# Optimization experiments

Hardware: AMD Instinct MI355X
Metric: run time of the kernel (lower is better)

The kernel has to match this reference:

```python
import jax, jax.numpy as jnp
import numpy as np

B, M, TP2, H, K, S = 64, 1, 1024, 256, 128, 1024
EPS = 2.220446049250313e-16  # numpy.finfo(float).eps


def setup_inputs() -> dict:
    key = jax.random.key(0)
    ks = jax.random.split(key, 12)
    inp = {
        'event': jax.random.randint(ks[0], (B, M, TP2), 0, K + 3),
        'dtime': jax.random.uniform(ks[1], (B, M, TP2), jnp.float32),
        'post': jax.random.uniform(ks[2], (B, M), jnp.float32),
        'duration': jax.random.uniform(ks[3], (B, M), jnp.float32),
        'dtime_sampling': jax.random.uniform(ks[4], (B, M, S), jnp.float32),
        'index_of_hidden_sampling': jax.random.randint(ks[5], (B, M, S), 0, B * M * (TP2 - 1)),
        'mask_sampling': jnp.ones((B, M, S), jnp.float32),
        # learned parameters
        'Emb': jax.random.normal(ks[6], (K + 3, H), jnp.float32) * 0.05,
        'W': jax.random.normal(ks[7], (7 * H, 2 * H), jnp.float32) * (1.0 / np.sqrt(2 * H)),
        'b': jnp.zeros((7 * H,), jnp.float32),
        'Wl': jax.random.normal(ks[8], (K, H), jnp.float32) * (1.0 / np.sqrt(H)),
    }
    return inp


def reference(event, dtime, post, duration, dtime_sampling, index_of_hidden_sampling,
              mask_sampling, Emb, W, b, Wl):
    Bs, Ms, Tp2 = event.shape
    Hd = Emb.shape[1]
    Tp1 = Tp2 - 1
    emb = Emb[event[:, :, :-1]]            # (B,M,T+1,H)
    dts = dtime[:, :, 1:]                  # (B,M,T+1)
    xs = (jnp.moveaxis(emb, 2, 0), jnp.moveaxis(dts, 2, 0))

    def step(carry, x):
        h, c, cbar = carry
        e, dt = x
        z = jnp.concatenate([e, h], axis=-1) @ W.T + b  # (B,M,7H)
        gi, gf, go, gz, gib, gfb, gd = jnp.split(z, 7, axis=-1)
        gi, gf, go = jax.nn.sigmoid(gi), jax.nn.sigmoid(gf), jax.nn.sigmoid(go)
        gib, gfb = jax.nn.sigmoid(gib), jax.nn.sigmoid(gfb)
        zc = jnp.tanh(gz)
        gd = jax.nn.softplus(gd)  # beta = 1
        c_i = gf * c + gi * zc
        cbar_i = gfb * cbar + gib * zc
        h_plus = go * jnp.tanh(c_i)  # decay with dtime = 0
        c_next = cbar_i + (c_i - cbar_i) * jnp.exp(-gd * dt[..., None])
        h_next = go * jnp.tanh(c_next)
        return (h_next, c_next, cbar_i), (c_i, cbar_i, gd, go, h_next)

    init = tuple(jnp.zeros((Bs, Ms, Hd), dtime.dtype) for _ in range(3))
    _, outs = jax.lax.scan(step, init, xs)
    all_c, all_cb, all_gd, all_go, all_h = (jnp.moveaxis(a, 0, 2) for a in outs)  # (B,M,T+1,H)

    # target + mask (getTarget)
    Kn = Wl.shape[0]
    tgt_raw = event[:, :, 1:]
    mask_complete = (tgt_raw < Kn).astype(dtime.dtype)
    tgt = jnp.where(tgt_raw < Kn, tgt_raw, 0)

    # log-intensity at events (getLogLambda)
    lam = jax.nn.softplus(all_h @ Wl.T)                        # (B,M,T+1,K)
    log_lam = jnp.log(lam + EPS)
    log_lam_tgt = jnp.take_along_axis(log_lam, tgt[..., None], axis=3)[..., 0] * mask_complete

    # sampled states (getSampledStates)
    idx = index_of_hidden_sampling.reshape(-1)
    Sn = dtime_sampling.shape[2]
    gather = lambda a: a.reshape(Bs * Ms * Tp1, Hd)[idx].reshape(Bs, Ms, Sn, Hd)
    cs, cbs, gds, gos = gather(all_c), gather(all_cb), gather(all_gd), gather(all_go)
    c_samp = cbs + (cs - cbs) * jnp.exp(-gds * dtime_sampling[..., None])
    hy = gos * jnp.tanh(c_samp)

    # MC integral (getIntegral)
    lam_s = jax.nn.softplus(hy @ Wl.T).sum(3)                  # (B,M,S)
    lam_mean = (lam_s * mask_sampling).sum(2) / mask_sampling.sum(2)
    integral = lam_mean * duration

    # complete log-likelihood per (batch, particle)
    loglik = log_lam_tgt.sum(2) - integral                     # (B,M)
    return loglik
```

## Files before the change

kernel.cpp:

```cpp
#include <hip/hip_runtime.h>
#include <hip/hip_fp16.h>
#include <cstdint>
#include <cstddef>

#define EPSF 2.220446049250313e-16f

#define Bn   64
#define TP2n 1024
#define Tn   1023
#define Hn   256
#define H7n  1792
#define Kn   128
#define NEn  131

typedef _Float16 f16x2 __attribute__((ext_vector_type(2)));
typedef unsigned uintx4 __attribute__((ext_vector_type(4)));

__device__ __forceinline__ f16x2 u2h(unsigned u) { return __builtin_bit_cast(f16x2, u); }
__device__ __forceinline__ f16x2 f2h(float f)    { return __builtin_bit_cast(f16x2, f); }

__device__ __forceinline__ int sdot4f(unsigned a, unsigned b, int c) {
#if __has_builtin(__builtin_amdgcn_sdot4)
  return __builtin_amdgcn_sdot4((int)a, (int)b, c, false);
#else
  int r = c;
#pragma unroll
  for (int i = 0; i < 4; ++i) {
    int av = ((int)(a << (24 - 8 * i))) >> 24;
    int bv = ((int)(b << (24 - 8 * i))) >> 24;
    r += av * bv;
  }
  return r;
#endif
}

__device__ __forceinline__ float sigmf(float x) { return 1.f / (1.f + __expf(-x)); }

__device__ __forceinline__ float tanhfast(float x) {
  float t = __expf(2.f * fabsf(x));
  float r = 1.f - 2.f / (t + 1.f);
  return copysignf(r, x);
}

__device__ __forceinline__ float softplusf(float x) {
  return fmaxf(x, 0.f) + log1pf(__expf(-fabsf(x)));
}

__device__ __host__ __forceinline__ int orig_row(int rp) {
  int role = rp / 448, i = rp % 448;
  return (i >> 6) * 256 + 64 * role + (i & 63);
}

__global__ __launch_bounds__(256) void k_ew(
    const float* __restrict__ Emb, const float* __restrict__ W,
    const float* __restrict__ bvec, float* __restrict__ EW) {
  const int e = blockIdx.x;
  const int chunk = blockIdx.y;
  const int tid = threadIdx.x;
  __shared__ float es[Hn];
  es[tid] = Emb[e * Hn + tid];
  __syncthreads();
  const int wv = tid >> 6, l = tid & 63;
  float4 ev = reinterpret_cast<const float4*>(es)[l];
  for (int i = 0; i < 28; ++i) {
    int rp = chunk * 112 + wv * 28 + i;
    int r = orig_row(rp);
    float4 wf = *reinterpret_cast<const float4*>(W + (size_t)r * 512 + 4 * l);
    float s = wf.x * ev.x + wf.y * ev.y + wf.z * ev.z + wf.w * ev.w;
#pragma unroll
    for (int off = 32; off; off >>= 1) s += __shfl_down(s, off);
    if (l == 0) EW[e * H7n + rp] = bvec[r] + s;
  }
}

__global__ __launch_bounds__(64) void k_wq8(const float* __restrict__ W,
                                            unsigned* __restrict__ wq,
                                            float* __restrict__ sc) {
  const int rp = blockIdx.x;
  const int r  = orig_row(rp);
  const int j  = threadIdx.x;
  const float* wr = W + (size_t)r * 512 + 256;
  float4 wv = *reinterpret_cast<const float4*>(wr + 4 * j);
  float m = fmaxf(fmaxf(fabsf(wv.x), fabsf(wv.y)),
                  fmaxf(fabsf(wv.z), fabsf(wv.w)));
#pragma unroll
  for (int off = 32; off; off >>= 1) m = fmaxf(m, __shfl_xor(m, off));
  float inv = (m > 0.f) ? 127.f / m : 0.f;
  float v[4] = {wv.x, wv.y, wv.z, wv.w};
  unsigned d = 0;
#pragma unroll
  for (int q = 0; q < 4; ++q) {
    float s = fminf(fmaxf(v[q] * inv, -127.f), 127.f);
    unsigned byte = (unsigned)((int)rintf(s)) & 255u;
    d |= byte << (8 * q);
  }
  wq[(size_t)rp * 64 + j] = d;
  if (j == 0) sc[rp] = m / (127.f * 127.f);
}

__global__ __launch_bounds__(64) void k_wlq(const float* __restrict__ Wl,
                                            unsigned* __restrict__ wlq,
                                            float* __restrict__ scl) {
  const int r = blockIdx.x;
  const int j = threadIdx.x;
  const float* row = Wl + (size_t)r * Hn;
  float4 v = reinterpret_cast<const float4*>(row)[j];
  float m = fmaxf(fmaxf(fabsf(v.x), fabsf(v.y)),
                  fmaxf(fabsf(v.z), fabsf(v.w)));
#pragma unroll
  for (int off = 32; off; off >>= 1) m = fmaxf(m, __shfl_xor(m, off));
  float inv = (m > 0.f) ? 127.f / m : 0.f;
  float vv[4] = {v.x, v.y, v.z, v.w};
  unsigned d = 0;
#pragma unroll
  for (int qi = 0; qi < 4; ++qi) {
    unsigned byte = (unsigned)((int)rintf(
        fminf(fmaxf(vv[qi] * inv, -127.f), 127.f))) & 255u;
    d |= byte << (8 * qi);
  }
  wlq[(((size_t)(j >> 2)) * 128 + r) * 4 + (j & 3)] = d;
  if (j == 0) scl[r] = m / (127.f * 127.f);
}

__global__ void k_init(float* __restrict__ acc, unsigned* __restrict__ hx) {
  int i = threadIdx.x;
  if (i < 192) acc[i] = 0.f;
  for (int k = i; k < Bn * 128; k += 1024) hx[k] = 1u;
}

__global__ __launch_bounds__(448) void k_scan(
    const int* __restrict__ event, const float* __restrict__ dtime,
    const float* __restrict__ EW, const unsigned* __restrict__ wq,
    const float* __restrict__ sc, unsigned* __restrict__ hx,
    uint2* __restrict__ state) {
  const int x = blockIdx.x;
  const int xcd = x & 7, q = x >> 3;
  const int b = xcd * 8 + (q >> 2);
  const int role = q & 3;
  const int tid = threadIdx.x;
  const int row = role * 448 + tid;

  __shared__ float    zbuf[448];
  __shared__ uintx4   hds8q[16];
  __shared__ int      ev_s[TP2n];
  __shared__ float    dt_s[TP2n];
  unsigned* hds8 = reinterpret_cast<unsigned*>(hds8q);

  const uintx4* wp = reinterpret_cast<const uintx4*>(wq) + (size_t)row * 16;
  const float  sc_r = sc[row];
  unsigned* hxb = hx + (size_t)b * 128;

  for (int i = tid; i < TP2n; i += 448) {
    ev_s[i] = event[b * TP2n + i];
    dt_s[i] = dtime[b * TP2n + i];
  }
  if (tid < 64) hds8[tid] = 0u;
  __syncthreads();

  float c_r = 0.f, cb_r = 0.f;
  const int j_u = 64 * role + tid;
  float ew_pf = EW[(size_t)ev_s[0] * H7n + row];

  for (int t = 0; t < Tn; ++t) {
    float ewc = ew_pf;
    ew_pf = EW[(size_t)ev_s[t + 1] * H7n + row];

    int acc0 = 0, acc1 = 0, acc2 = 0, acc3 = 0;
#pragma unroll
    for (int i = 0; i < 16; ++i) {
      uintx4 ww = wp[i];
      uintx4 hh = hds8q[i];
      acc0 = sdot4f(ww[0], hh[0], acc0);
      acc1 = sdot4f(ww[1], hh[1], acc1);
      acc2 = sdot4f(ww[2], hh[2], acc2);
      acc3 = sdot4f(ww[3], hh[3], acc3);
    }
    zbuf[tid] = ewc + sc_r * (float)((acc0 + acc1) + (acc2 + acc3));
    __syncthreads();

    const unsigned parQ = (unsigned)(t & 1);
    const unsigned tauQ = (unsigned)((t >> 1) & 1);

    if (tid < 64) {
      float gi  = sigmf(zbuf[tid]);
      float gf  = sigmf(zbuf[64 + tid]);
      float go  = sigmf(zbuf[128 + tid]);
      float zc  = tanhfast(zbuf[192 + tid]);
      float gib = sigmf(zbuf[256 + tid]);
      float gfb = sigmf(zbuf[320 + tid]);
      float gd  = softplusf(zbuf[384 + tid]);
      float dt  = dt_s[t + 1];
      float ci  = gf * c_r + gi * zc;
      float cbi = gfb * cb_r + gib * zc;
      float cn  = cbi + (ci - cbi) * __expf(-gd * dt);
      float hn  = go * tanhfast(cn);
      c_r = cn; cb_r = cbi;
      unsigned bq = (unsigned)((int)rintf(
                        fminf(fmaxf(hn * 127.f, -127.f), 127.f))) & 255u;
      unsigned u0 = __shfl(bq, 4 * (tid & 15));
      unsigned u1 = __shfl(bq, 4 * (tid & 15) + 1);
      unsigned u2 = __shfl(bq, 4 * (tid & 15) + 2);
      unsigned u3 = __shfl(bq, 4 * (tid & 15) + 3);
      if (tid < 16) {
        unsigned d = u0 | (u1 << 8) | (u2 << 16) | (u3 << 24);
        hds8[16 * role + tid] = d;
        if (t < Tn - 1)
          __hip_atomic_store(hxb + parQ * 64 + 16 * role + tid,
                             (d & 0xFFFFFFFEu) | tauQ,
                             __ATOMIC_RELAXED, __HIP_MEMORY_SCOPE_AGENT);
      }
      f16x2 p0; p0[0] = (_Float16)ci; p0[1] = (_Float16)cbi;
      f16x2 p1; p1[0] = (_Float16)gd; p1[1] = (_Float16)go;
      uint2 o;
      o.x = __builtin_bit_cast(unsigned, p0);
      o.y = __builtin_bit_cast(unsigned, p1);
      state[((size_t)b * Tn + t) * Hn + j_u] = o;
    } else if (tid < 112 && t < Tn - 1) {
      int k  = tid - 64;
      int rr = (role + 1 + (k >> 4)) & 3;
      int m  = 16 * rr + (k & 15);
      unsigned v;
      do {
        v = __hip_atomic_load(hxb + parQ * 64 + m, __ATOMIC_RELAXED,
                              __HIP_MEMORY_SCOPE_AGENT);
      } while ((v & 1u) != tauQ);
      hds8[m] = v;
    }
    __syncthreads();
  }
}

__global__ __launch_bounds__(256) void k_post(
    const uint2* __restrict__ state, const int* __restrict__ event,
    const float* __restrict__ dtime, const float* __restrict__ Wl,
    float* __restrict__ loglik_sum) {
  const int b = blockIdx.y;
  const int wave = threadIdx.x >> 6;
  const int lane = threadIdx.x & 63;
  __shared__ float part[4];
  float acc = 0.f;
  for (int i = 0; i < 16; ++i) {
    const int t = blockIdx.x * 64 + wave * 16 + i;
    if (t >= Tn) break;
    const int tgt = event[b * TP2n + t + 1];
    if (tgt >= Kn) continue;
    const float dtv = dtime[b * TP2n + t + 1];
    const uint2* srow = state + ((size_t)b * Tn + t) * Hn;
    uint4 sA = *reinterpret_cast<const uint4*>(srow + lane * 4);
    uint4 sB = *reinterpret_cast<const uint4*>(srow + lane * 4 + 2);
    float4 wl = *reinterpret_cast<const float4*>(Wl + tgt * Hn + lane * 4);
    float h[4];
#pragma unroll
    for (int qq = 0; qq < 4; ++qq) {
      unsigned lo = (qq == 0) ? sA.x : (qq == 1) ? sA.z : (qq == 2) ? sB.x : sB.z;
      unsigned hi = (qq == 0) ? sA.y : (qq == 1) ? sA.w : (qq == 2) ? sB.y : sB.w;
      f16x2 p0 = u2h(lo), p1 = u2h(hi);
      float c = p0[0], cb = p0[1], gd = p1[0], go = p1[1];
      float cs = cb + (c - cb) * __expf(-gd * dtv);
      h[qq] = go * tanhfast(cs);
    }
    float d = h[0] * wl.x + h[1] * wl.y + h[2] * wl.z + h[3] * wl.w;
#pragma unroll
    for (int off = 32; off; off >>= 1) d += __shfl_down(d, off);
    if (lane == 0) acc += __logf(softplusf(d) + EPSF);
  }
  if (lane == 0) part[wave] = acc;
  __syncthreads();
  if (threadIdx.x == 0)
    atomicAdd(&loglik_sum[b], part[0] + part[1] + part[2] + part[3]);
}

__global__ __launch_bounds__(128) void k_samp(
    const uint2* __restrict__ state, const unsigned* __restrict__ wlq,
    const float* __restrict__ scl,
    const int* __restrict__ sidx, const float* __restrict__ sdt,
    const float* __restrict__ smask,
    float* __restrict__ lam_acc, float* __restrict__ mask_acc) {
  const int blk = blockIdx.x;
  const int b = blk >> 4;
  const int base = (b << 10) + (blk & 15) * 64;
  const int tid = threadIdx.x;

  __shared__ uintx4 wlt4[2048];
  __shared__ uintx4 hq4[16];
  __shared__ float  red[2];

  const uintx4* wg = reinterpret_cast<const uintx4*>(wlq);
  for (int i = tid; i < 2048; i += 128) wlt4[i] = wg[i];
  const float sc_row = scl[tid];
  float accl = 0.f, accm = 0.f;

  int   row = sidx[base];
  float dtv = sdt[base];
  float mk  = smask[base];
  uint4 st = *reinterpret_cast<const uint4*>(state + (size_t)row * Hn + 2 * tid);
  __syncthreads();

  for (int s = 0; s < 64; ++s) {
    f16x2 p0 = u2h(st.x), p1 = u2h(st.y);
    f16x2 q0 = u2h(st.z), q1 = u2h(st.w);
    float cs0 = (float)p0[1] + ((float)p0[0] - (float)p0[1]) * __expf(-(float)p1[0] * dtv);
    float cs1 = (float)q0[1] + ((float)q0[0] - (float)q0[1]) * __expf(-(float)q1[0] * dtv);
    float h0 = (float)p1[1] * tanhfast(cs0);
    float h1 = (float)q1[1] * tanhfast(cs1);
    unsigned i0 = (unsigned)((int)rintf(fminf(fmaxf(h0 * 127.f, -127.f), 127.f))) & 255u;
    unsigned i1 = (unsigned)((int)rintf(fminf(fmaxf(h1 * 127.f, -127.f), 127.f))) & 255u;
    unsigned p = i0 | (i1 << 8);
    unsigned pn = __shfl(p, tid + 1);
    if (!(tid & 1))
      reinterpret_cast<unsigned*>(hq4)[tid >> 1] = p | (pn << 16);

    uint4 st_n = st; float dt_n = dtv, mk_n = mk;
    if (s < 63) {
      int sg = base + s + 1;
      int r2 = sidx[sg];
      dt_n = sdt[sg];
      mk_n = smask[sg];
      st_n = *reinterpret_cast<const uint4*>(state + (size_t)r2 * Hn + 2 * tid);
    }
    __syncthreads();

    int acc = 0;
#pragma unroll
    for (int kg = 0; kg < 16; ++kg) {
      uintx4 w4 = wlt4[kg * 128 + tid];
      uintx4 h4 = hq4[kg];
      acc = sdot4f(w4[0], h4[0], acc);
      acc = sdot4f(w4[1], h4[1], acc);
      acc = sdot4f(w4[2], h4[2], acc);
      acc = sdot4f(w4[3], h4[3], acc);
    }
    float lam = softplusf(sc_row * (float)acc);
#pragma unroll
    for (int off = 32; off; off >>= 1) lam += __shfl_down(lam, off);
    if ((tid & 63) == 0) red[tid >> 6] = lam;
    __syncthreads();
    if (tid == 0) {
      accl += (red[0] + red[1]) * mk;
      accm += mk;
    }
    st = st_n; dtv = dt_n; mk = mk_n;
  }
  if (tid == 0) {
    atomicAdd(&lam_acc[b], accl);
    atomicAdd(&mask_acc[b], accm);
  }
}

__global__ void k_final(const float* __restrict__ loglik_sum,
                        const float* __restrict__ lam_acc,
                        const float* __restrict__ mask_acc,
                        const float* __restrict__ duration,
                        float* __restrict__ out) {
  int b = threadIdx.x;
  if (b < Bn) out[b] = loglik_sum[b] - (lam_acc[b] / mask_acc[b]) * duration[b];
}

extern "C" void kernel_launch(void* const* d_in, const int* in_sizes, int n_in,
                              void* d_out, int out_size, void* d_ws, size_t ws_size,
                              hipStream_t stream) {
  const int*   event    = (const int*)d_in[0];
  const float* dtime    = (const float*)d_in[1];
  const float* duration = (const float*)d_in[3];
  const float* sdt      = (const float*)d_in[4];
  const int*   sidx     = (const int*)d_in[5];
  const float* smask    = (const float*)d_in[6];
  const float* Emb      = (const float*)d_in[7];
  const float* W        = (const float*)d_in[8];
  const float* bv       = (const float*)d_in[9];
  const float* Wl       = (const float*)d_in[10];

  char* ws = (char*)d_ws;
  float*    EW         = (float*)(ws + 0);
  unsigned* wq         = (unsigned*)(ws + (1u << 20));
  float*    lam_acc    = (float*)(ws + (2u << 20));
  float*    mask_acc   = lam_acc + 64;
  float*    loglik_sum = lam_acc + 128;
  unsigned* hx         = (unsigned*)(ws + (2u << 20) + 8192);
  float*    sc         = (float*)(ws + (2u << 20) + 49152);
  unsigned* wlq        = (unsigned*)(ws + (2u << 20) + 131072);
  float*    scl        = (float*)(ws + (2u << 20) + 196608);
  uint2*    state      = (uint2*)(ws + (4u << 20));

  k_ew<<<dim3(NEn, 16), dim3(256), 0, stream>>>(Emb, W, bv, EW);
  k_wq8<<<dim3(H7n), dim3(64), 0, stream>>>(W, wq, sc);
  k_wlq<<<dim3(Kn), dim3(64), 0, stream>>>(Wl, wlq, scl);
  k_init<<<dim3(1), dim3(1024), 0, stream>>>(lam_acc, hx);
  k_scan<<<dim3(256), dim3(448), 0, stream>>>(event, dtime, EW, wq, sc, hx,
                                              state);
  k_post<<<dim3(16, 64), dim3(256), 0, stream>>>(state, event, dtime, Wl,
                                                 loglik_sum);
  k_samp<<<dim3(1024), dim3(128), 0, stream>>>(state, wlq, scl, sidx, sdt,
                                               smask, lam_acc, mask_acc);
  k_final<<<dim3(1), dim3(64), 0, stream>>>(loglik_sum, lam_acc, mask_acc,
                                            duration, (float*)d_out);
}
```

Baseline: 1.997 ms.

## Overlap local-slice hidden dot product with remote hidden exchange wait

Each block now computes the dot product over its own quarter of the hidden vector as soon as its own gate wave publishes it, signalled through a workgroup-scope LDS flag. This runs while other waves are still polling for the remote quarters from peer blocks. The weights for the local slice are kept in registers, and the gate wave raises its scheduling priority for the critical path. The cost is extra register pressure and spin-waiting on the LDS flag by every wave each step.

```diff
diff --git a/kernel.cpp b/kernel.cpp
--- a/kernel.cpp
+++ b/kernel.cpp
@@ -144,44 +144,58 @@
   __shared__ uintx4   hds8q[16];
   __shared__ int      ev_s[TP2n];
   __shared__ float    dt_s[TP2n];
+  __shared__ int      hflag;
   unsigned* hds8 = reinterpret_cast<unsigned*>(hds8q);
 
   const uintx4* wp = reinterpret_cast<const uintx4*>(wq) + (size_t)row * 16;
   const float  sc_r = sc[row];
   unsigned* hxb = hx + (size_t)b * 128;
 
+  const uintx4 wo0 = wp[4 * role + 0];
+  const uintx4 wo1 = wp[4 * role + 1];
+  const uintx4 wo2 = wp[4 * role + 2];
+  const uintx4 wo3 = wp[4 * role + 3];
+
   for (int i = tid; i < TP2n; i += 448) {
     ev_s[i] = event[b * TP2n + i];
     dt_s[i] = dtime[b * TP2n + i];
   }
   if (tid < 64) hds8[tid] = 0u;
+  if (tid == 0) hflag = 0;
   __syncthreads();
 
   float c_r = 0.f, cb_r = 0.f;
   const int j_u = 64 * role + tid;
   float ew_pf = EW[(size_t)ev_s[0] * H7n + row];
+  int aloc = 0;
 
   for (int t = 0; t < Tn; ++t) {
     float ewc = ew_pf;
     ew_pf = EW[(size_t)ev_s[t + 1] * H7n + row];
 
-    int acc0 = 0, acc1 = 0, acc2 = 0, acc3 = 0;
-#pragma unroll
-    for (int i = 0; i < 16; ++i) {
-      uintx4 ww = wp[i];
-      uintx4 hh = hds8q[i];
-      acc0 = sdot4f(ww[0], hh[0], acc0);
-      acc1 = sdot4f(ww[1], hh[1], acc1);
-      acc2 = sdot4f(ww[2], hh[2], acc2);
-      acc3 = sdot4f(ww[3], hh[3], acc3);
-    }
-    zbuf[tid] = ewc + sc_r * (float)((acc0 + acc1) + (acc2 + acc3));
+    int a0 = 0, a1 = 0, a2 = 0, a3 = 0;
+#pragma unroll
+    for (int kk = 1; kk <= 3; ++kk) {
+      const int rr = (role + kk) & 3;
+#pragma unroll
+      for (int g = 0; g < 4; ++g) {
+        const int i = 4 * rr + g;
+        uintx4 ww = wp[i];
+        uintx4 hh = hds8q[i];
+        a0 = sdot4f(ww[0], hh[0], a0);
+        a1 = sdot4f(ww[1], hh[1], a1);
+        a2 = sdot4f(ww[2], hh[2], a2);
+        a3 = sdot4f(ww[3], hh[3], a3);
+      }
+    }
+    zbuf[tid] = ewc + sc_r * (float)(((a0 + a1) + (a2 + a3)) + aloc);
     __syncthreads();
 
     const unsigned parQ = (unsigned)(t & 1);
     const unsigned tauQ = (unsigned)((t >> 1) & 1);
 
     if (tid < 64) {
+      __builtin_amdgcn_s_setprio(1);
       float gi  = sigmf(zbuf[tid]);
       float gf  = sigmf(zbuf[64 + tid]);
       float go  = sigmf(zbuf[128 + tid]);
@@ -201,14 +215,18 @@
       unsigned u1 = __shfl(bq, 4 * (tid & 15) + 1);
       unsigned u2 = __shfl(bq, 4 * (tid & 15) + 2);
       unsigned u3 = __shfl(bq, 4 * (tid & 15) + 3);
+      unsigned d = u0 | (u1 << 8) | (u2 << 16) | (u3 << 24);
       if (tid < 16) {
-        unsigned d = u0 | (u1 << 8) | (u2 << 16) | (u3 << 24);
         hds8[16 * role + tid] = d;
         if (t < Tn - 1)
           __hip_atomic_store(hxb + parQ * 64 + 16 * role + tid,
                              (d & 0xFFFFFFFEu) | tauQ,
                              __ATOMIC_RELAXED, __HIP_MEMORY_SCOPE_AGENT);
       }
+      __builtin_amdgcn_s_setprio(0);
+      if (tid == 0 && t < Tn - 1)
+        __hip_atomic_store(&hflag, t + 1, __ATOMIC_RELEASE,
+                           __HIP_MEMORY_SCOPE_WORKGROUP);
       f16x2 p0; p0[0] = (_Float16)ci; p0[1] = (_Float16)cbi;
       f16x2 p1; p1[0] = (_Float16)gd; p1[1] = (_Float16)go;
       uint2 o;
@@ -225,6 +243,25 @@
                               __HIP_MEMORY_SCOPE_AGENT);
       } while ((v & 1u) != tauQ);
       hds8[m] = v;
+    }
+
+    if (t < Tn - 1) {
+      while (__hip_atomic_load(&hflag, __ATOMIC_ACQUIRE,
+                               __HIP_MEMORY_SCOPE_WORKGROUP) <= t) {}
+      uintx4 h0 = hds8q[4 * role + 0];
+      uintx4 h1 = hds8q[4 * role + 1];
+      uintx4 h2 = hds8q[4 * role + 2];
+      uintx4 h3 = hds8q[4 * role + 3];
+      int l0 = 0, l1 = 0, l2 = 0, l3 = 0;
+      l0 = sdot4f(wo0[0], h0[0], l0); l1 = sdot4f(wo0[1], h0[1], l1);
+      l2 = sdot4f(wo0[2], h0[2], l2); l3 = sdot4f(wo0[3], h0[3], l3);
+      l0 = sdot4f(wo1[0], h1[0], l0); l1 = sdot4f(wo1[1], h1[1], l1);
+      l2 = sdot4f(wo1[2], h1[2], l2); l3 = sdot4f(wo1[3], h1[3], l3);
+      l0 = sdot4f(wo2[0], h2[0], l0); l1 = sdot4f(wo2[1], h2[1], l1);
+      l2 = sdot4f(wo2[2], h2[2], l2); l3 = sdot4f(wo2[3], h2[3], l3);
+      l0 = sdot4f(wo3[0], h3[0], l0); l1 = sdot4f(wo3[1], h3[1], l1);
+      l2 = sdot4f(wo3[2], h3[2], l2); l3 = sdot4f(wo3[3], h3[3], l3);
+      aloc = (l0 + l1) + (l2 + l3);
     }
     __syncthreads();
   }
```

Measured after the change: 2.050 ms. +2.7%, slower.
